# Kernel tuning notes

Hardware: AMD Instinct MI355X
Metric: run time of the kernel (lower is better)

## Reference

```python
import jax, jax.numpy as jnp
import numpy as np

N, IN_DIM, H, ATT_DIM, OUT_DIM = 4096, 512, 8, 64, 64
ATT_BIAS = 0.5


def setup_inputs() -> dict:
    key = jax.random.key(0)
    ks = jax.random.split(key, 12)
    s_in = 1.0 / np.sqrt(IN_DIM)
    s_o = 1.0 / np.sqrt(H * OUT_DIM)
    return {
        "Q": jax.random.normal(ks[0], (N, IN_DIM), jnp.float32),
        "K": jax.random.normal(ks[1], (N, IN_DIM), jnp.float32),
        "V": jax.random.normal(ks[2], (N, IN_DIM), jnp.float32),
        "adj": jax.random.uniform(ks[3], (N, N), jnp.float32),
        "WQ": jax.random.normal(ks[4], (IN_DIM, H * ATT_DIM), jnp.float32) * s_in,
        "bQ": jnp.zeros((H * ATT_DIM,), jnp.float32),
        "WK": jax.random.normal(ks[5], (IN_DIM, H * ATT_DIM), jnp.float32) * s_in,
        "bK": jnp.zeros((H * ATT_DIM,), jnp.float32),
        "WV": jax.random.normal(ks[6], (IN_DIM, H * OUT_DIM), jnp.float32) * s_in,
        "bV": jnp.zeros((H * OUT_DIM,), jnp.float32),
        "WO": jax.random.normal(ks[7], (H * OUT_DIM, OUT_DIM), jnp.float32) * s_o,
        "bO": jnp.zeros((OUT_DIM,), jnp.float32),
    }


def reference(Q, K, V, adj, WQ, bQ, WK, bK, WV, bV, WO, bO):
    scale = ATT_DIM ** -0.5
    q = (Q @ WQ + bQ).reshape(N, H, ATT_DIM)   # [N,H,d]
    k = (K @ WK + bK).reshape(N, H, ATT_DIM)   # [N,H,d]
    v = (V @ WV + bV).reshape(N, H, OUT_DIM)   # [N,H,e]
    # scaled QK^T per head: [H,N,N]
    scores = jnp.einsum("nhd,mhd->hnm", q * scale, k)
    # sigmoid -> bias subtract -> +0.1*adj -> softmax over keys
    scores = jax.nn.sigmoid(scores) - ATT_BIAS + 0.1 * adj[None, :, :]
    attn = jax.nn.softmax(scores, axis=2)
    # attend values (dropout p=0 => identity), concat heads, project
    out = jnp.einsum("hnm,mhe->nhe", attn, v).reshape(N, H * OUT_DIM)
    return out @ WO + bO
```

## Files before the change

kernel.cpp:

```cpp
#include <hip/hip_runtime.h>
#include <hip/hip_bf16.h>

#define N_TOK  4096
#define HD     512
#define NH     8
#define NSPLIT 4
#define QBLK   128
#define NT     ((N_TOK / NSPLIT) / 64)

typedef short v8s __attribute__((ext_vector_type(8)));
typedef float v4f __attribute__((ext_vector_type(4)));
typedef float v16f __attribute__((ext_vector_type(16)));
typedef unsigned short u16;

#define QSCALE   0.18033688011112042f
#define ADJ2     0.14426950408889634f
#define EA0 0.999410f
#define EA1 1.016220f
#define EA2 0.423120f
#define EA3 0.279120f

__device__ __forceinline__ float bf2f(u16 x) {
  union { unsigned int u; float f; } c; c.u = ((unsigned int)x) << 16; return c.f;
}
__device__ __forceinline__ u16 f2bf(float f) {
  union { float f; unsigned int u; } c; c.f = f;
  return (u16)((c.u + 0x7fffu + ((c.u >> 16) & 1u)) >> 16);
}
__device__ __forceinline__ float fast_exp2(float x) {
#if __has_builtin(__builtin_amdgcn_exp2f)
  return __builtin_amdgcn_exp2f(x);
#else
  return exp2f(x);
#endif
}
__device__ __forceinline__ unsigned int pk_bf16(float a, float b) {
  union { __hip_bfloat162 h; unsigned int u; } c;
  c.h = __float22bfloat162_rn(make_float2(a, b));
  return c.u;
}

typedef __attribute__((address_space(1))) const char gchar;
typedef __attribute__((address_space(3))) char lchar;
__device__ __forceinline__ void glds16(const void* g, void* l) {
  __builtin_amdgcn_global_load_lds((gchar*)g, (lchar*)l, 16, 0, 0);
}
__device__ __forceinline__ void plswap(unsigned int& a, unsigned int& b) {
  asm volatile("v_permlane32_swap_b32 %0, %1" : "+v"(a), "+v"(b));
}

__device__ __forceinline__ bool detect_f32(const u16* __restrict__ q) {
  int l = threadIdx.x & 63;
  u16 e = q[2 * l];
  float x = bf2f(e);
  int ex = (e >> 7) & 0xFF;
  float ax = fabsf(x);
  bool ok = (ex != 0xFF) && (ax < 64.f) && (ax > 1e-30f);
  unsigned long long m = __ballot(ok);
  return __popcll(m) < 48;
}
__device__ __forceinline__ float bias_ld(const void* b, int i, bool f32) {
  return f32 ? ((const float*)b)[i] : bf2f(((const u16*)b)[i]);
}

__global__ __launch_bounds__(256) void conv_adjE_k(const void* __restrict__ adj, u16* __restrict__ adjE,
                                                   const u16* __restrict__ Qdet) {
  bool f32 = detect_f32(Qdet);
  int i = blockIdx.x * 256 + threadIdx.x;
  float4 f;
  if (f32) {
    f = ((const float4*)adj)[i];
  } else {
    short4 v = ((const short4*)adj)[i];
    f.x = bf2f((u16)v.x); f.y = bf2f((u16)v.y); f.z = bf2f((u16)v.z); f.w = bf2f((u16)v.w);
  }
  unsigned int d0 = pk_bf16(fast_exp2(f.x * ADJ2), fast_exp2(f.y * ADJ2));
  unsigned int d1 = pk_bf16(fast_exp2(f.z * ADJ2), fast_exp2(f.w * ADJ2));
  ((uint2*)adjE)[i] = make_uint2(d0, d1);
}

__global__ __launch_bounds__(256) void tr_w_k(const void* W0, const void* W1, const void* W2, const void* W3,
                                              u16* t0, u16* t1, u16* t2, u16* t3,
                                              const u16* __restrict__ Qdet) {
  bool f32 = detect_f32(Qdet);
  int z = blockIdx.z;
  const void* in; u16* out; int C;
  if (z == 0)      { in = W0; out = t0; C = 512; }
  else if (z == 1) { in = W1; out = t1; C = 512; }
  else if (z == 2) { in = W2; out = t2; C = 512; }
  else             { in = W3; out = t3; C = 64; if (blockIdx.y) return; }
  const int R = 512;
  __shared__ __align__(16) u16 tile[64][72];
  const int r0 = blockIdx.x * 64, c0 = blockIdx.y * 64;
  const int t = threadIdx.x;
#pragma unroll
  for (int rep = 0; rep < 2; ++rep) {
    int idx = (t + rep * 256) * 8;
    int r = idx >> 6, c = idx & 63;
    if (f32) {
      const float* sp = (const float*)in + (size_t)(r0 + r) * C + (c0 + c);
      float4 a = *(const float4*)sp, b = *(const float4*)(sp + 4);
      uint4 q = make_uint4(pk_bf16(a.x, a.y), pk_bf16(a.z, a.w),
                           pk_bf16(b.x, b.y), pk_bf16(b.z, b.w));
      *(uint4*)&tile[r][c] = q;
    } else {
      *(v8s*)&tile[r][c] = *(const v8s*)((const u16*)in + (size_t)(r0 + r) * C + (c0 + c));
    }
  }
  __syncthreads();
#pragma unroll
  for (int rep = 0; rep < 2; ++rep) {
    int idx = (t + rep * 256) * 8;
    int oc = idx >> 6, orr = idx & 63;
    u16 tmp[8];
#pragma unroll
    for (int j = 0; j < 8; ++j) tmp[j] = tile[orr + j][oc];
    *(v8s*)(out + (size_t)(c0 + oc) * R + (r0 + orr)) = *(v8s*)tmp;
  }
}

__global__ __launch_bounds__(256) void gemm_qkv_k(const void* A0, const void* A1, const void* A2,
                                                  const u16* __restrict__ t0, const u16* __restrict__ t1,
                                                  const u16* __restrict__ t2,
                                                  const void* b0, const void* b1, const void* b2,
                                                  u16* __restrict__ qb, u16* __restrict__ kb,
                                                  u16* __restrict__ vtb) {
  __shared__ __align__(16) u16 As[64][72];
  __shared__ __align__(16) u16 Bs[64][72];
  bool f32 = detect_f32((const u16*)A0);
  int z = blockIdx.z;
  const void* Araw = (z == 0) ? A0 : (z == 1) ? A1 : A2;
  const u16* Bt    = (z == 0) ? t0 : (z == 1) ? t1 : t2;
  const void* bias = (z == 0) ? b0 : (z == 1) ? b1 : b2;
  const bool vt = (z == 2);
  const int i0 = blockIdx.x * 64, j0 = blockIdx.y * 64;
  const int t = threadIdx.x, w = t >> 6, l = t & 63, quad = l >> 4, l15 = l & 15;
  v4f acc[4] = {};
  for (int k0 = 0; k0 < 512; k0 += 64) {
#pragma unroll
    for (int rep = 0; rep < 2; ++rep) {
      int idx = (t + rep * 256) * 8;
      int r = idx >> 6, c = idx & 63;
      if (f32) {
        const float* sp = (const float*)Araw + (size_t)(i0 + r) * 512 + k0 + c;
        float4 fa = *(const float4*)sp, fb = *(const float4*)(sp + 4);
        uint4 q = make_uint4(pk_bf16(fa.x, fa.y), pk_bf16(fa.z, fa.w),
                             pk_bf16(fb.x, fb.y), pk_bf16(fb.z, fb.w));
        *(uint4*)&As[r][c] = q;
      } else {
        *(v8s*)&As[r][c] = *(const v8s*)((const u16*)Araw + (size_t)(i0 + r) * 512 + k0 + c);
      }
      *(v8s*)&Bs[r][c] = *(const v8s*)(Bt + (size_t)(j0 + r) * 512 + k0 + c);
    }
    __syncthreads();
    if (vt) {
#pragma unroll
      for (int h = 0; h < 2; ++h) {
        v8s a = *(const v8s*)&As[w * 16 + l15][h * 32 + quad * 8];
#pragma unroll
        for (int cb = 0; cb < 4; ++cb) {
          v8s b = *(const v8s*)&Bs[cb * 16 + l15][h * 32 + quad * 8];
          acc[cb] = __builtin_amdgcn_mfma_f32_16x16x32_bf16(b, a, acc[cb], 0, 0, 0);
        }
      }
    } else {
#pragma unroll
      for (int h = 0; h < 2; ++h) {
        v8s a = *(const v8s*)&As[w * 16 + l15][h * 32 + quad * 8];
#pragma unroll
        for (int cb = 0; cb < 4; ++cb) {
          v8s b = *(const v8s*)&Bs[cb * 16 + l15][h * 32 + quad * 8];
          acc[cb] = __builtin_amdgcn_mfma_f32_16x16x32_bf16(a, b, acc[cb], 0, 0, 0);
        }
      }
    }
    __syncthreads();
  }
  if (vt) {
#pragma unroll
    for (int cb = 0; cb < 4; ++cb) {
#pragma unroll
      for (int r = 0; r < 4; ++r) {
        int jj = j0 + cb * 16 + quad * 4 + r;
        int ii = i0 + w * 16 + l15;
        vtb[(size_t)jj * N_TOK + ii] = f2bf(acc[cb][r] + bias_ld(bias, jj, f32));
      }
    }
  } else {
    const float oscale = (z == 0) ? QSCALE : 1.0f;
    u16* C = (z == 0) ? qb : kb;
#pragma unroll
    for (int cb = 0; cb < 4; ++cb) {
      int col = j0 + cb * 16 + l15;
      float bv = bias_ld(bias, col, f32);
#pragma unroll
      for (int r = 0; r < 4; ++r) {
        int row = i0 + w * 16 + quad * 4 + r;
        C[(size_t)row * HD + col] = f2bf((acc[cb][r] + bv) * oscale);
      }
    }
  }
}

__global__ __launch_bounds__(256, 4) void attn_kernel(const u16* __restrict__ qb, const u16* __restrict__ kb,
                                                      const u16* __restrict__ vtb, const u16* __restrict__ adjE,
                                                      u16* __restrict__ Opart, float* __restrict__ Lpart) {
  __shared__ __align__(16) u16 Ks[2][64 * 64];
  __shared__ __align__(16) u16 Vs[2][64 * 64];
  const int i0 = blockIdx.x * QBLK, h64 = blockIdx.y * 64, z = blockIdx.z;
  const int t = threadIdx.x, w = t >> 6, l = t & 63;
  const int il = l & 31, h2 = l >> 5, il7 = il & 7;
  const int iRow = i0 + w * 32 + il;

  v8s qf[4];
#pragma unroll
  for (int c = 0; c < 4; ++c)
    qf[c] = *(const v8s*)(qb + (size_t)iRow * HD + h64 + 16 * c + 8 * h2);

  const u16* adjRow = adjE + (size_t)iRow * N_TOK + 4 * h2;

  const int srow = l >> 3;
  const int scol = ((l & 7) ^ srow) * 8;
  const int ldsrow = 16 * w;

  v16f oacc0 = {}, oacc1 = {};
  float lsum = 0.f;
  const int m_begin = z * (N_TOK / NSPLIT);

#pragma unroll
  for (int n = 0; n < 2; ++n) {
    int r = ldsrow + 8 * n + srow;
    glds16(kb + (size_t)(m_begin + r) * HD + h64 + scol, &Ks[0][(ldsrow + 8 * n) * 64]);
    glds16(vtb + (size_t)(h64 + r) * N_TOK + m_begin + scol, &Vs[0][(ldsrow + 8 * n) * 64]);
  }
  __syncthreads();

  int buf = 0;
  for (int mt = 0; mt < NT; ++mt) {
    const int m0 = m_begin + mt * 64;
    if (mt + 1 < NT) {
      const int m1 = m0 + 64;
#pragma unroll
      for (int n = 0; n < 2; ++n) {
        int r = ldsrow + 8 * n + srow;
        glds16(kb + (size_t)(m1 + r) * HD + h64 + scol, &Ks[buf ^ 1][(ldsrow + 8 * n) * 64]);
        glds16(vtb + (size_t)(h64 + r) * N_TOK + m1 + scol, &Vs[buf ^ 1][(ldsrow + 8 * n) * 64]);
      }
    }
    const u16* Kb = &Ks[buf][0];
    const u16* Vb = &Vs[buf][0];

#pragma unroll
    for (int mh = 0; mh < 2; ++mh) {
      uint2 av[4];
#pragma unroll
      for (int rq = 0; rq < 4; ++rq)
        av[rq] = *(const uint2*)(adjRow + m0 + 32 * mh + 8 * rq);

      v16f macc = {};
      __builtin_amdgcn_s_setprio(1);
#pragma unroll
      for (int c = 0; c < 4; ++c) {
        v8s kf = *(const v8s*)(Kb + (32 * mh + il) * 64 + (((2 * c + h2) ^ il7) * 8));
        macc = __builtin_amdgcn_mfma_f32_32x32x16_bf16(kf, qf[c], macc, 0, 0, 0);
      }
      __builtin_amdgcn_s_setprio(0);

      float p[16];
#pragma unroll
      for (int rq = 0; rq < 4; ++rq) {
        union { unsigned int u; float f; } e0, e1, e2, e3;
        e0.u = av[rq].x << 16; e1.u = av[rq].x & 0xFFFF0000u;
        e2.u = av[rq].y << 16; e3.u = av[rq].y & 0xFFFF0000u;
        float r0 = __builtin_amdgcn_rcpf(1.f + fast_exp2(-macc[4 * rq + 0]));
        float r1 = __builtin_amdgcn_rcpf(1.f + fast_exp2(-macc[4 * rq + 1]));
        float r2 = __builtin_amdgcn_rcpf(1.f + fast_exp2(-macc[4 * rq + 2]));
        float r3 = __builtin_amdgcn_rcpf(1.f + fast_exp2(-macc[4 * rq + 3]));
        float p0 = e0.f * fmaf(fmaf(fmaf(EA3, r0, EA2), r0, EA1), r0, EA0);
        float p1 = e1.f * fmaf(fmaf(fmaf(EA3, r1, EA2), r1, EA1), r1, EA0);
        float p2 = e2.f * fmaf(fmaf(fmaf(EA3, r2, EA2), r2, EA1), r2, EA0);
        float p3 = e3.f * fmaf(fmaf(fmaf(EA3, r3, EA2), r3, EA1), r3, EA0);
        lsum += (p0 + p1) + (p2 + p3);
        p[4 * rq + 0] = p0; p[4 * rq + 1] = p1; p[4 * rq + 2] = p2; p[4 * rq + 3] = p3;
      }

      v8s pf[2];
#pragma unroll
      for (int sub = 0; sub < 2; ++sub) {
        unsigned int u0 = pk_bf16(p[8 * sub + 0], p[8 * sub + 1]);
        unsigned int u1 = pk_bf16(p[8 * sub + 2], p[8 * sub + 3]);
        unsigned int u2 = pk_bf16(p[8 * sub + 4], p[8 * sub + 5]);
        unsigned int u3 = pk_bf16(p[8 * sub + 6], p[8 * sub + 7]);
        plswap(u0, u2); plswap(u1, u3);
        union { uint4 q; v8s v; } pu;
        pu.q = make_uint4(u0, u1, u2, u3);
        pf[sub] = pu.v;
      }

      __builtin_amdgcn_s_setprio(1);
#pragma unroll
      for (int sub = 0; sub < 2; ++sub) {
        const int mc = 2 * mh + sub;
        v8s vf0 = *(const v8s*)(Vb + (il) * 64      + (((2 * mc + h2) ^ il7) * 8));
        v8s vf1 = *(const v8s*)(Vb + (32 + il) * 64 + (((2 * mc + h2) ^ il7) * 8));
        oacc0 = __builtin_amdgcn_mfma_f32_32x32x16_bf16(pf[sub], vf0, oacc0, 0, 0, 0);
        oacc1 = __builtin_amdgcn_mfma_f32_32x32x16_bf16(pf[sub], vf1, oacc1, 0, 0, 0);
      }
      __builtin_amdgcn_s_setprio(0);
    }
    __syncthreads();
    buf ^= 1;
  }

  lsum += __shfl_xor(lsum, 32);
  if (l < 32)
    Lpart[((size_t)z * N_TOK + i0 + 32 * w + il) * NH + blockIdx.y] = lsum;

#pragma unroll
  for (int r = 0; r < 16; ++r) {
    int i_local = (r & 3) + 8 * (r >> 2) + 4 * h2;
    size_t row = (size_t)z * N_TOK + i0 + 32 * w + i_local;
    u16* op = Opart + row * HD + h64 + il;
    op[0]  = f2bf(oacc0[r]);
    op[32] = f2bf(oacc1[r]);
  }
}

__global__ __launch_bounds__(256) void gemm_bt(const u16* __restrict__ Opart, const float* __restrict__ Lpart,
                                               const u16* __restrict__ Bt, const void* bias,
                                               void* __restrict__ C, const u16* __restrict__ Qdet) {
  __shared__ __align__(16) u16 As[64][72];
  __shared__ __align__(16) u16 Bs[64][72];
  bool f32 = detect_f32(Qdet);
  const int i0 = blockIdx.x * 64;
  const int t = threadIdx.x, w = t >> 6, l = t & 63, quad = l >> 4, l15 = l & 15;
  v4f acc[4] = {};
  for (int k0 = 0; k0 < 512; k0 += 64) {
    const int h = k0 >> 6;
#pragma unroll
    for (int rep = 0; rep < 2; ++rep) {
      int idx = (t + rep * 256) * 8;
      int r = idx >> 6, c = idx & 63;
      float lv = 0.f;
#pragma unroll
      for (int s = 0; s < NSPLIT; ++s) lv += Lpart[((size_t)s * N_TOK + i0 + r) * NH + h];
      float rl = __builtin_amdgcn_rcpf(lv);
      float vals[8] = {};
#pragma unroll
      for (int s = 0; s < NSPLIT; ++s) {
        v8s ov = *(const v8s*)(Opart + ((size_t)s * N_TOK + i0 + r) * HD + k0 + c);
#pragma unroll
        for (int j = 0; j < 8; ++j) vals[j] += bf2f((u16)ov[j]);
      }
      uint4 q = make_uint4(pk_bf16(vals[0] * rl, vals[1] * rl), pk_bf16(vals[2] * rl, vals[3] * rl),
                           pk_bf16(vals[4] * rl, vals[5] * rl), pk_bf16(vals[6] * rl, vals[7] * rl));
      *(uint4*)&As[r][c] = q;
      *(v8s*)&Bs[r][c] = *(const v8s*)(Bt + (size_t)r * 512 + k0 + c);
    }
    __syncthreads();
#pragma unroll
    for (int h2 = 0; h2 < 2; ++h2) {
      v8s a = *(const v8s*)&As[w * 16 + l15][h2 * 32 + quad * 8];
#pragma unroll
      for (int cb = 0; cb < 4; ++cb) {
        v8s b = *(const v8s*)&Bs[cb * 16 + l15][h2 * 32 + quad * 8];
        acc[cb] = __builtin_amdgcn_mfma_f32_16x16x32_bf16(a, b, acc[cb], 0, 0, 0);
      }
    }
    __syncthreads();
  }
#pragma unroll
  for (int cb = 0; cb < 4; ++cb) {
    int col = cb * 16 + l15;
    float bv = bias_ld(bias, col, f32);
#pragma unroll
    for (int r = 0; r < 4; ++r) {
      int row = i0 + w * 16 + quad * 4 + r;
      float v = acc[cb][r] + bv;
      size_t idx = (size_t)row * 64 + col;
      if (f32) ((float*)C)[idx] = v;
      else     ((u16*)C)[idx] = f2bf(v);
    }
  }
}

extern "C" void kernel_launch(void* const* d_in, const int* in_sizes, int n_in,
                              void* d_out, int out_size, void* d_ws, size_t ws_size,
                              hipStream_t stream) {
  (void)in_sizes; (void)n_in; (void)out_size; (void)ws_size;
  const void* Q   = d_in[0];
  const void* K   = d_in[1];
  const void* V   = d_in[2];
  const void* adj = d_in[3];
  const void* WQ  = d_in[4];
  const void* bQ  = d_in[5];
  const void* WK  = d_in[6];
  const void* bK  = d_in[7];
  const void* WV  = d_in[8];
  const void* bV  = d_in[9];
  const void* WO  = d_in[10];
  const void* bO  = d_in[11];
  const u16* Qdet = (const u16*)Q;

  char* p = (char*)d_ws;
  auto alloc = [&](size_t bytes) { char* r = p; p += (bytes + 255) & ~(size_t)255; return r; };
  const size_t SZ = (size_t)N_TOK * HD * 2;

  u16* adjE    = (u16*)alloc((size_t)N_TOK * N_TOK * 2);
  u16* qb      = (u16*)alloc(SZ);
  u16* kb      = (u16*)alloc(SZ);
  u16* vtb     = (u16*)alloc(SZ);
  u16* Opart   = (u16*)alloc((size_t)NSPLIT * SZ);
  float* Lpart = (float*)alloc((size_t)NSPLIT * N_TOK * NH * 4);
  u16* tQ      = (u16*)alloc((size_t)512 * 512 * 2);
  u16* tK      = (u16*)alloc((size_t)512 * 512 * 2);
  u16* tV      = (u16*)alloc((size_t)512 * 512 * 2);
  u16* tO      = (u16*)alloc((size_t)64 * 512 * 2);

  dim3 b256(256);
  conv_adjE_k<<<dim3(16384), b256, 0, stream>>>(adj, adjE, Qdet);
  tr_w_k<<<dim3(8, 8, 4), b256, 0, stream>>>(WQ, WK, WV, WO, tQ, tK, tV, tO, Qdet);
  gemm_qkv_k<<<dim3(64, 8, 3), b256, 0, stream>>>(Q, K, V, tQ, tK, tV,
                                                  bQ, bK, bV, qb, kb, vtb);
  attn_kernel<<<dim3(N_TOK / QBLK, NH, NSPLIT), b256, 0, stream>>>(qb, kb, vtb, adjE, Opart, Lpart);
  gemm_bt<<<dim3(64, 1), b256, 0, stream>>>(Opart, Lpart, tO, bO, d_out, Qdet);
}
```

Before: 263.9 us.

## Fuse adjacency exp conversion into attention kernel and software-pipeline tile phases

Removes the separate pre-pass that converted adj into a bf16 exp2 table and instead reads raw adj (fp32 or bf16) directly inside the attention kernel. The kernel computes exp2(L2E*sigmoid + adj*ADJ2) with a real exp instead of the polynomial times a precomputed exp. The tile loop is restructured so K fragments, adj values and V fragments are loaded ahead and the two 32-key halves interleave. The intent is to avoid the extra pass writing and reading a 32 MB table. In exchange each of the 8 head blocks rereads fp32 adj, doubling adj bytes per read, and occupancy drops to 3 waves per SIMD.

```diff
diff --git a/kernel.cpp b/kernel.cpp
--- a/kernel.cpp
+++ b/kernel.cpp
@@ -15,10 +15,7 @@
 
 #define QSCALE   0.18033688011112042f
 #define ADJ2     0.14426950408889634f
-#define EA0 0.999410f
-#define EA1 1.016220f
-#define EA2 0.423120f
-#define EA3 0.279120f
+#define L2E      1.4426950408889634f
 
 __device__ __forceinline__ float bf2f(u16 x) {
   union { unsigned int u; float f; } c; c.u = ((unsigned int)x) << 16; return c.f;
@@ -61,22 +58,6 @@
 }
 __device__ __forceinline__ float bias_ld(const void* b, int i, bool f32) {
   return f32 ? ((const float*)b)[i] : bf2f(((const u16*)b)[i]);
-}
-
-__global__ __launch_bounds__(256) void conv_adjE_k(const void* __restrict__ adj, u16* __restrict__ adjE,
-                                                   const u16* __restrict__ Qdet) {
-  bool f32 = detect_f32(Qdet);
-  int i = blockIdx.x * 256 + threadIdx.x;
-  float4 f;
-  if (f32) {
-    f = ((const float4*)adj)[i];
-  } else {
-    short4 v = ((const short4*)adj)[i];
-    f.x = bf2f((u16)v.x); f.y = bf2f((u16)v.y); f.z = bf2f((u16)v.z); f.w = bf2f((u16)v.w);
-  }
-  unsigned int d0 = pk_bf16(fast_exp2(f.x * ADJ2), fast_exp2(f.y * ADJ2));
-  unsigned int d1 = pk_bf16(fast_exp2(f.z * ADJ2), fast_exp2(f.w * ADJ2));
-  ((uint2*)adjE)[i] = make_uint2(d0, d1);
 }
 
 __global__ __launch_bounds__(256) void tr_w_k(const void* W0, const void* W1, const void* W2, const void* W3,
@@ -202,11 +183,52 @@
   }
 }
 
-__global__ __launch_bounds__(256, 4) void attn_kernel(const u16* __restrict__ qb, const u16* __restrict__ kb,
-                                                      const u16* __restrict__ vtb, const u16* __restrict__ adjE,
+__device__ __forceinline__ void ew_phase(const v16f& macc, const uint4* av, bool f32m,
+                                         float& lsum, v8s* pf) {
+  unsigned int ua[8];
+#pragma unroll
+  for (int rq = 0; rq < 4; ++rq) {
+    float a0, a1, a2, a3;
+    if (f32m) {
+      union { unsigned int u; float f; } c0, c1, c2, c3;
+      c0.u = av[rq].x; c1.u = av[rq].y; c2.u = av[rq].z; c3.u = av[rq].w;
+      a0 = c0.f * ADJ2; a1 = c1.f * ADJ2; a2 = c2.f * ADJ2; a3 = c3.f * ADJ2;
+    } else {
+      union { unsigned int u; float f; } e0, e1, e2, e3;
+      e0.u = av[rq].x << 16; e1.u = av[rq].x & 0xFFFF0000u;
+      e2.u = av[rq].y << 16; e3.u = av[rq].y & 0xFFFF0000u;
+      a0 = e0.f * ADJ2; a1 = e1.f * ADJ2; a2 = e2.f * ADJ2; a3 = e3.f * ADJ2;
+    }
+    float r0 = __builtin_amdgcn_rcpf(1.f + fast_exp2(-macc[4 * rq + 0]));
+    float r1 = __builtin_amdgcn_rcpf(1.f + fast_exp2(-macc[4 * rq + 1]));
+    float r2 = __builtin_amdgcn_rcpf(1.f + fast_exp2(-macc[4 * rq + 2]));
+    float r3 = __builtin_amdgcn_rcpf(1.f + fast_exp2(-macc[4 * rq + 3]));
+    float p0 = fast_exp2(fmaf(L2E, r0, a0));
+    float p1 = fast_exp2(fmaf(L2E, r1, a1));
+    float p2 = fast_exp2(fmaf(L2E, r2, a2));
+    float p3 = fast_exp2(fmaf(L2E, r3, a3));
+    lsum += (p0 + p1) + (p2 + p3);
+    ua[2 * rq]     = pk_bf16(p0, p1);
+    ua[2 * rq + 1] = pk_bf16(p2, p3);
+  }
+#pragma unroll
+  for (int sub = 0; sub < 2; ++sub) {
+    unsigned int u0 = ua[4 * sub + 0], u1 = ua[4 * sub + 1];
+    unsigned int u2 = ua[4 * sub + 2], u3 = ua[4 * sub + 3];
+    plswap(u0, u2); plswap(u1, u3);
+    union { uint4 q; v8s v; } pu;
+    pu.q = make_uint4(u0, u1, u2, u3);
+    pf[sub] = pu.v;
+  }
+}
+
+__global__ __launch_bounds__(256, 3) void attn_kernel(const u16* __restrict__ qb, const u16* __restrict__ kb,
+                                                      const u16* __restrict__ vtb, const void* __restrict__ adj,
+                                                      const u16* __restrict__ Qdet,
                                                       u16* __restrict__ Opart, float* __restrict__ Lpart) {
   __shared__ __align__(16) u16 Ks[2][64 * 64];
   __shared__ __align__(16) u16 Vs[2][64 * 64];
+  const bool f32m = detect_f32(Qdet);
   const int i0 = blockIdx.x * QBLK, h64 = blockIdx.y * 64, z = blockIdx.z;
   const int t = threadIdx.x, w = t >> 6, l = t & 63;
   const int il = l & 31, h2 = l >> 5, il7 = il & 7;
@@ -217,7 +239,8 @@
   for (int c = 0; c < 4; ++c)
     qf[c] = *(const v8s*)(qb + (size_t)iRow * HD + h64 + 16 * c + 8 * h2);
 
-  const u16* adjRow = adjE + (size_t)iRow * N_TOK + 4 * h2;
+  const float* aRowF = (const float*)adj + (size_t)iRow * N_TOK + 4 * h2;
+  const u16*   aRowH = (const u16*)adj  + (size_t)iRow * N_TOK + 4 * h2;
 
   const int srow = l >> 3;
   const int scol = ((l & 7) ^ srow) * 8;
@@ -238,6 +261,31 @@
   int buf = 0;
   for (int mt = 0; mt < NT; ++mt) {
     const int m0 = m_begin + mt * 64;
+    const u16* Kb = &Ks[buf][0];
+    const u16* Vb = &Vs[buf][0];
+
+    v8s kfA[4];
+#pragma unroll
+    for (int c = 0; c < 4; ++c)
+      kfA[c] = *(const v8s*)(Kb + il * 64 + (((2 * c + h2) ^ il7) * 8));
+
+    uint4 av0[4], av1[4];
+    if (f32m) {
+#pragma unroll
+      for (int rq = 0; rq < 4; ++rq) {
+        av0[rq] = *(const uint4*)(aRowF + m0 + 8 * rq);
+        av1[rq] = *(const uint4*)(aRowF + m0 + 32 + 8 * rq);
+      }
+    } else {
+#pragma unroll
+      for (int rq = 0; rq < 4; ++rq) {
+        uint2 t0 = *(const uint2*)(aRowH + m0 + 8 * rq);
+        uint2 t1 = *(const uint2*)(aRowH + m0 + 32 + 8 * rq);
+        av0[rq].x = t0.x; av0[rq].y = t0.y; av0[rq].z = 0; av0[rq].w = 0;
+        av1[rq].x = t1.x; av1[rq].y = t1.y; av1[rq].z = 0; av1[rq].w = 0;
+      }
+    }
+
     if (mt + 1 < NT) {
       const int m1 = m0 + 64;
 #pragma unroll
@@ -247,67 +295,57 @@
         glds16(vtb + (size_t)(h64 + r) * N_TOK + m1 + scol, &Vs[buf ^ 1][(ldsrow + 8 * n) * 64]);
       }
     }
-    const u16* Kb = &Ks[buf][0];
-    const u16* Vb = &Vs[buf][0];
-
-#pragma unroll
-    for (int mh = 0; mh < 2; ++mh) {
-      uint2 av[4];
-#pragma unroll
-      for (int rq = 0; rq < 4; ++rq)
-        av[rq] = *(const uint2*)(adjRow + m0 + 32 * mh + 8 * rq);
-
-      v16f macc = {};
-      __builtin_amdgcn_s_setprio(1);
-#pragma unroll
-      for (int c = 0; c < 4; ++c) {
-        v8s kf = *(const v8s*)(Kb + (32 * mh + il) * 64 + (((2 * c + h2) ^ il7) * 8));
-        macc = __builtin_amdgcn_mfma_f32_32x32x16_bf16(kf, qf[c], macc, 0, 0, 0);
-      }
-      __builtin_amdgcn_s_setprio(0);
-
-      float p[16];
-#pragma unroll
-      for (int rq = 0; rq < 4; ++rq) {
-        union { unsigned int u; float f; } e0, e1, e2, e3;
-        e0.u = av[rq].x << 16; e1.u = av[rq].x & 0xFFFF0000u;
-        e2.u = av[rq].y << 16; e3.u = av[rq].y & 0xFFFF0000u;
-        float r0 = __builtin_amdgcn_rcpf(1.f + fast_exp2(-macc[4 * rq + 0]));
-        float r1 = __builtin_amdgcn_rcpf(1.f + fast_exp2(-macc[4 * rq + 1]));
-        float r2 = __builtin_amdgcn_rcpf(1.f + fast_exp2(-macc[4 * rq + 2]));
-        float r3 = __builtin_amdgcn_rcpf(1.f + fast_exp2(-macc[4 * rq + 3]));
-        float p0 = e0.f * fmaf(fmaf(fmaf(EA3, r0, EA2), r0, EA1), r0, EA0);
-        float p1 = e1.f * fmaf(fmaf(fmaf(EA3, r1, EA2), r1, EA1), r1, EA0);
-        float p2 = e2.f * fmaf(fmaf(fmaf(EA3, r2, EA2), r2, EA1), r2, EA0);
-        float p3 = e3.f * fmaf(fmaf(fmaf(EA3, r3, EA2), r3, EA1), r3, EA0);
-        lsum += (p0 + p1) + (p2 + p3);
-        p[4 * rq + 0] = p0; p[4 * rq + 1] = p1; p[4 * rq + 2] = p2; p[4 * rq + 3] = p3;
-      }
-
-      v8s pf[2];
-#pragma unroll
-      for (int sub = 0; sub < 2; ++sub) {
-        unsigned int u0 = pk_bf16(p[8 * sub + 0], p[8 * sub + 1]);
-        unsigned int u1 = pk_bf16(p[8 * sub + 2], p[8 * sub + 3]);
-        unsigned int u2 = pk_bf16(p[8 * sub + 4], p[8 * sub + 5]);
-        unsigned int u3 = pk_bf16(p[8 * sub + 6], p[8 * sub + 7]);
-        plswap(u0, u2); plswap(u1, u3);
-        union { uint4 q; v8s v; } pu;
-        pu.q = make_uint4(u0, u1, u2, u3);
-        pf[sub] = pu.v;
-      }
-
-      __builtin_amdgcn_s_setprio(1);
-#pragma unroll
-      for (int sub = 0; sub < 2; ++sub) {
-        const int mc = 2 * mh + sub;
-        v8s vf0 = *(const v8s*)(Vb + (il) * 64      + (((2 * mc + h2) ^ il7) * 8));
-        v8s vf1 = *(const v8s*)(Vb + (32 + il) * 64 + (((2 * mc + h2) ^ il7) * 8));
-        oacc0 = __builtin_amdgcn_mfma_f32_32x32x16_bf16(pf[sub], vf0, oacc0, 0, 0, 0);
-        oacc1 = __builtin_amdgcn_mfma_f32_32x32x16_bf16(pf[sub], vf1, oacc1, 0, 0, 0);
-      }
-      __builtin_amdgcn_s_setprio(0);
-    }
+
+    v16f macc = {};
+    __builtin_amdgcn_s_setprio(1);
+#pragma unroll
+    for (int c = 0; c < 4; ++c)
+      macc = __builtin_amdgcn_mfma_f32_32x32x16_bf16(kfA[c], qf[c], macc, 0, 0, 0);
+    __builtin_amdgcn_s_setprio(0);
+
+    v8s kfB[4];
+#pragma unroll
+    for (int c = 0; c < 4; ++c)
+      kfB[c] = *(const v8s*)(Kb + (32 + il) * 64 + (((2 * c + h2) ^ il7) * 8));
+    v8s vf[4];
+#pragma unroll
+    for (int sub = 0; sub < 2; ++sub) {
+      vf[2 * sub]     = *(const v8s*)(Vb + il * 64        + (((2 * sub + h2) ^ il7) * 8));
+      vf[2 * sub + 1] = *(const v8s*)(Vb + (32 + il) * 64 + (((2 * sub + h2) ^ il7) * 8));
+    }
+
+    v8s pf[2];
+    ew_phase(macc, av0, f32m, lsum, pf);
+    __builtin_amdgcn_s_setprio(1);
+#pragma unroll
+    for (int sub = 0; sub < 2; ++sub) {
+      oacc0 = __builtin_amdgcn_mfma_f32_32x32x16_bf16(pf[sub], vf[2 * sub], oacc0, 0, 0, 0);
+      oacc1 = __builtin_amdgcn_mfma_f32_32x32x16_bf16(pf[sub], vf[2 * sub + 1], oacc1, 0, 0, 0);
+    }
+    __builtin_amdgcn_s_setprio(0);
+
+    v16f macc2 = {};
+    __builtin_amdgcn_s_setprio(1);
+#pragma unroll
+    for (int c = 0; c < 4; ++c)
+      macc2 = __builtin_amdgcn_mfma_f32_32x32x16_bf16(kfB[c], qf[c], macc2, 0, 0, 0);
+    __builtin_amdgcn_s_setprio(0);
+
+#pragma unroll
+    for (int sub = 0; sub < 2; ++sub) {
+      vf[2 * sub]     = *(const v8s*)(Vb + il * 64        + (((2 * (2 + sub) + h2) ^ il7) * 8));
+      vf[2 * sub + 1] = *(const v8s*)(Vb + (32 + il) * 64 + (((2 * (2 + sub) + h2) ^ il7) * 8));
+    }
+
+    ew_phase(macc2, av1, f32m, lsum, pf);
+    __builtin_amdgcn_s_setprio(1);
+#pragma unroll
+    for (int sub = 0; sub < 2; ++sub) {
+      oacc0 = __builtin_amdgcn_mfma_f32_32x32x16_bf16(pf[sub], vf[2 * sub], oacc0, 0, 0, 0);
+      oacc1 = __builtin_amdgcn_mfma_f32_32x32x16_bf16(pf[sub], vf[2 * sub + 1], oacc1, 0, 0, 0);
+    }
+    __builtin_amdgcn_s_setprio(0);
+
     __syncthreads();
     buf ^= 1;
   }
@@ -406,7 +444,6 @@
   auto alloc = [&](size_t bytes) { char* r = p; p += (bytes + 255) & ~(size_t)255; return r; };
   const size_t SZ = (size_t)N_TOK * HD * 2;
 
-  u16* adjE    = (u16*)alloc((size_t)N_TOK * N_TOK * 2);
   u16* qb      = (u16*)alloc(SZ);
   u16* kb      = (u16*)alloc(SZ);
   u16* vtb     = (u16*)alloc(SZ);
@@ -418,10 +455,9 @@
   u16* tO      = (u16*)alloc((size_t)64 * 512 * 2);
 
   dim3 b256(256);
-  conv_adjE_k<<<dim3(16384), b256, 0, stream>>>(adj, adjE, Qdet);
   tr_w_k<<<dim3(8, 8, 4), b256, 0, stream>>>(WQ, WK, WV, WO, tQ, tK, tV, tO, Qdet);
   gemm_qkv_k<<<dim3(64, 8, 3), b256, 0, stream>>>(Q, K, V, tQ, tK, tV,
                                                   bQ, bK, bV, qb, kb, vtb);
-  attn_kernel<<<dim3(N_TOK / QBLK, NH, NSPLIT), b256, 0, stream>>>(qb, kb, vtb, adjE, Opart, Lpart);
+  attn_kernel<<<dim3(N_TOK / QBLK, NH, NSPLIT), b256, 0, stream>>>(qb, kb, vtb, adj, Qdet, Opart, Lpart);
   gemm_bt<<<dim3(64, 1), b256, 0, stream>>>(Opart, Lpart, tO, bO, d_out, Qdet);
 }
```

After: 363.1 us. 37.6% more time.

## Deepen attention split, prefetch adjacency with explicit vmcnt pipeline, separate combine kernel

Applied to the files above, without the earlier changes.

Doubles the key-dimension split so the attention grid has twice as many blocks. The attention loop is restructured into a two-stage software pipeline: adjacency loads are prefetched into registers along with the K/V LDS loads, and hand-placed vmcnt waits and barriers replace the old per-tile syncthreads. The split-combine and normalisation move out of the 64-block output GEMM into a wide standalone combine kernel. This aims to hide global-load latency and raise parallelism, at the cost of more partial-output traffic, an extra launch and more register pressure.

```diff
diff --git a/kernel.cpp b/kernel.cpp
--- a/kernel.cpp
+++ b/kernel.cpp
@@ -4,7 +4,7 @@
 #define N_TOK  4096
 #define HD     512
 #define NH     8
-#define NSPLIT 4
+#define NSPLIT 8
 #define QBLK   128
 #define NT     ((N_TOK / NSPLIT) / 64)
 
@@ -48,6 +48,9 @@
 __device__ __forceinline__ void plswap(unsigned int& a, unsigned int& b) {
   asm volatile("v_permlane32_swap_b32 %0, %1" : "+v"(a), "+v"(b));
 }
+#define WAIT12 asm volatile("s_waitcnt vmcnt(12)" ::: "memory")
+#define WAIT0  asm volatile("s_waitcnt vmcnt(0)" ::: "memory")
+#define SBAR   __builtin_amdgcn_s_barrier()
 
 __device__ __forceinline__ bool detect_f32(const u16* __restrict__ q) {
   int l = threadIdx.x & 63;
@@ -202,6 +205,63 @@
   }
 }
 
+__device__ __forceinline__ void tile_compute(const u16* __restrict__ Kb, const u16* __restrict__ Vb,
+                                             const uint2* av, const v8s* qf,
+                                             v16f& oacc0, v16f& oacc1, float& lsum,
+                                             int il, int h2, int il7) {
+#pragma unroll
+  for (int mh = 0; mh < 2; ++mh) {
+    v16f macc = {};
+    __builtin_amdgcn_s_setprio(1);
+#pragma unroll
+    for (int c = 0; c < 4; ++c) {
+      v8s kf = *(const v8s*)(Kb + (32 * mh + il) * 64 + (((2 * c + h2) ^ il7) * 8));
+      macc = __builtin_amdgcn_mfma_f32_32x32x16_bf16(kf, qf[c], macc, 0, 0, 0);
+    }
+    __builtin_amdgcn_s_setprio(0);
+
+    unsigned int ua[8];
+#pragma unroll
+    for (int rq = 0; rq < 4; ++rq) {
+      uint2 a = av[4 * mh + rq];
+      union { unsigned int u; float f; } e0, e1, e2, e3;
+      e0.u = a.x << 16; e1.u = a.x & 0xFFFF0000u;
+      e2.u = a.y << 16; e3.u = a.y & 0xFFFF0000u;
+      float r0 = __builtin_amdgcn_rcpf(1.f + fast_exp2(-macc[4 * rq + 0]));
+      float r1 = __builtin_amdgcn_rcpf(1.f + fast_exp2(-macc[4 * rq + 1]));
+      float r2 = __builtin_amdgcn_rcpf(1.f + fast_exp2(-macc[4 * rq + 2]));
+      float r3 = __builtin_amdgcn_rcpf(1.f + fast_exp2(-macc[4 * rq + 3]));
+      float p0 = e0.f * fmaf(fmaf(fmaf(EA3, r0, EA2), r0, EA1), r0, EA0);
+      float p1 = e1.f * fmaf(fmaf(fmaf(EA3, r1, EA2), r1, EA1), r1, EA0);
+      float p2 = e2.f * fmaf(fmaf(fmaf(EA3, r2, EA2), r2, EA1), r2, EA0);
+      float p3 = e3.f * fmaf(fmaf(fmaf(EA3, r3, EA2), r3, EA1), r3, EA0);
+      lsum += (p0 + p1) + (p2 + p3);
+      ua[2 * rq]     = pk_bf16(p0, p1);
+      ua[2 * rq + 1] = pk_bf16(p2, p3);
+    }
+    v8s pf[2];
+#pragma unroll
+    for (int sub = 0; sub < 2; ++sub) {
+      unsigned int u0 = ua[4 * sub + 0], u1 = ua[4 * sub + 1];
+      unsigned int u2 = ua[4 * sub + 2], u3 = ua[4 * sub + 3];
+      plswap(u0, u2); plswap(u1, u3);
+      union { uint4 q; v8s v; } pu;
+      pu.q = make_uint4(u0, u1, u2, u3);
+      pf[sub] = pu.v;
+    }
+    __builtin_amdgcn_s_setprio(1);
+#pragma unroll
+    for (int sub = 0; sub < 2; ++sub) {
+      const int mc = 2 * mh + sub;
+      v8s vf0 = *(const v8s*)(Vb + il * 64        + (((2 * mc + h2) ^ il7) * 8));
+      v8s vf1 = *(const v8s*)(Vb + (32 + il) * 64 + (((2 * mc + h2) ^ il7) * 8));
+      oacc0 = __builtin_amdgcn_mfma_f32_32x32x16_bf16(pf[sub], vf0, oacc0, 0, 0, 0);
+      oacc1 = __builtin_amdgcn_mfma_f32_32x32x16_bf16(pf[sub], vf1, oacc1, 0, 0, 0);
+    }
+    __builtin_amdgcn_s_setprio(0);
+  }
+}
+
 __global__ __launch_bounds__(256, 4) void attn_kernel(const u16* __restrict__ qb, const u16* __restrict__ kb,
                                                       const u16* __restrict__ vtb, const u16* __restrict__ adjE,
                                                       u16* __restrict__ Opart, float* __restrict__ Lpart) {
@@ -215,7 +275,7 @@
   v8s qf[4];
 #pragma unroll
   for (int c = 0; c < 4; ++c)
-    qf[c] = *(const v8s*)(qb + (size_t)iRow * HD + h64 + 16 * c + 8 * h2);
+    qf[c] = *(const v8s*)(qb + (size_t)iRow * HD + 16 * c + 8 * h2 + h64);
 
   const u16* adjRow = adjE + (size_t)iRow * N_TOK + 4 * h2;
 
@@ -223,94 +283,61 @@
   const int scol = ((l & 7) ^ srow) * 8;
   const int ldsrow = 16 * w;
 
+#define ADJLD(AV, MM)                                                        \
+  _Pragma("unroll") for (int q_ = 0; q_ < 8; ++q_)                           \
+      AV[q_] = *(const uint2*)(adjRow + (MM) + 32 * (q_ >> 2) + 8 * (q_ & 3));
+#define STAGE(KB, VB, MM)                                                    \
+  _Pragma("unroll") for (int n_ = 0; n_ < 2; ++n_) {                         \
+    int r_ = ldsrow + 8 * n_ + srow;                                         \
+    glds16(kb + (size_t)((MM) + r_) * HD + h64 + scol,                       \
+           (u16*)(KB) + (ldsrow + 8 * n_) * 64);                             \
+    glds16(vtb + (size_t)(h64 + r_) * N_TOK + (MM) + scol,                   \
+           (u16*)(VB) + (ldsrow + 8 * n_) * 64);                             \
+  }
+
   v16f oacc0 = {}, oacc1 = {};
   float lsum = 0.f;
   const int m_begin = z * (N_TOK / NSPLIT);
-
-#pragma unroll
-  for (int n = 0; n < 2; ++n) {
-    int r = ldsrow + 8 * n + srow;
-    glds16(kb + (size_t)(m_begin + r) * HD + h64 + scol, &Ks[0][(ldsrow + 8 * n) * 64]);
-    glds16(vtb + (size_t)(h64 + r) * N_TOK + m_begin + scol, &Vs[0][(ldsrow + 8 * n) * 64]);
-  }
-  __syncthreads();
-
-  int buf = 0;
-  for (int mt = 0; mt < NT; ++mt) {
-    const int m0 = m_begin + mt * 64;
-    if (mt + 1 < NT) {
-      const int m1 = m0 + 64;
-#pragma unroll
-      for (int n = 0; n < 2; ++n) {
-        int r = ldsrow + 8 * n + srow;
-        glds16(kb + (size_t)(m1 + r) * HD + h64 + scol, &Ks[buf ^ 1][(ldsrow + 8 * n) * 64]);
-        glds16(vtb + (size_t)(h64 + r) * N_TOK + m1 + scol, &Vs[buf ^ 1][(ldsrow + 8 * n) * 64]);
-      }
-    }
-    const u16* Kb = &Ks[buf][0];
-    const u16* Vb = &Vs[buf][0];
-
-#pragma unroll
-    for (int mh = 0; mh < 2; ++mh) {
-      uint2 av[4];
-#pragma unroll
-      for (int rq = 0; rq < 4; ++rq)
-        av[rq] = *(const uint2*)(adjRow + m0 + 32 * mh + 8 * rq);
-
-      v16f macc = {};
-      __builtin_amdgcn_s_setprio(1);
-#pragma unroll
-      for (int c = 0; c < 4; ++c) {
-        v8s kf = *(const v8s*)(Kb + (32 * mh + il) * 64 + (((2 * c + h2) ^ il7) * 8));
-        macc = __builtin_amdgcn_mfma_f32_32x32x16_bf16(kf, qf[c], macc, 0, 0, 0);
-      }
-      __builtin_amdgcn_s_setprio(0);
-
-      float p[16];
-#pragma unroll
-      for (int rq = 0; rq < 4; ++rq) {
-        union { unsigned int u; float f; } e0, e1, e2, e3;
-        e0.u = av[rq].x << 16; e1.u = av[rq].x & 0xFFFF0000u;
-        e2.u = av[rq].y << 16; e3.u = av[rq].y & 0xFFFF0000u;
-        float r0 = __builtin_amdgcn_rcpf(1.f + fast_exp2(-macc[4 * rq + 0]));
-        float r1 = __builtin_amdgcn_rcpf(1.f + fast_exp2(-macc[4 * rq + 1]));
-        float r2 = __builtin_amdgcn_rcpf(1.f + fast_exp2(-macc[4 * rq + 2]));
-        float r3 = __builtin_amdgcn_rcpf(1.f + fast_exp2(-macc[4 * rq + 3]));
-        float p0 = e0.f * fmaf(fmaf(fmaf(EA3, r0, EA2), r0, EA1), r0, EA0);
-        float p1 = e1.f * fmaf(fmaf(fmaf(EA3, r1, EA2), r1, EA1), r1, EA0);
-        float p2 = e2.f * fmaf(fmaf(fmaf(EA3, r2, EA2), r2, EA1), r2, EA0);
-        float p3 = e3.f * fmaf(fmaf(fmaf(EA3, r3, EA2), r3, EA1), r3, EA0);
-        lsum += (p0 + p1) + (p2 + p3);
-        p[4 * rq + 0] = p0; p[4 * rq + 1] = p1; p[4 * rq + 2] = p2; p[4 * rq + 3] = p3;
-      }
-
-      v8s pf[2];
-#pragma unroll
-      for (int sub = 0; sub < 2; ++sub) {
-        unsigned int u0 = pk_bf16(p[8 * sub + 0], p[8 * sub + 1]);
-        unsigned int u1 = pk_bf16(p[8 * sub + 2], p[8 * sub + 3]);
-        unsigned int u2 = pk_bf16(p[8 * sub + 4], p[8 * sub + 5]);
-        unsigned int u3 = pk_bf16(p[8 * sub + 6], p[8 * sub + 7]);
-        plswap(u0, u2); plswap(u1, u3);
-        union { uint4 q; v8s v; } pu;
-        pu.q = make_uint4(u0, u1, u2, u3);
-        pf[sub] = pu.v;
-      }
-
-      __builtin_amdgcn_s_setprio(1);
-#pragma unroll
-      for (int sub = 0; sub < 2; ++sub) {
-        const int mc = 2 * mh + sub;
-        v8s vf0 = *(const v8s*)(Vb + (il) * 64      + (((2 * mc + h2) ^ il7) * 8));
-        v8s vf1 = *(const v8s*)(Vb + (32 + il) * 64 + (((2 * mc + h2) ^ il7) * 8));
-        oacc0 = __builtin_amdgcn_mfma_f32_32x32x16_bf16(pf[sub], vf0, oacc0, 0, 0, 0);
-        oacc1 = __builtin_amdgcn_mfma_f32_32x32x16_bf16(pf[sub], vf1, oacc1, 0, 0, 0);
-      }
-      __builtin_amdgcn_s_setprio(0);
-    }
-    __syncthreads();
-    buf ^= 1;
-  }
+  uint2 avA[8], avB[8];
+
+  ADJLD(avA, m_begin)
+  STAGE(Ks[0], Vs[0], m_begin)
+  ADJLD(avB, m_begin + 64)
+  STAGE(Ks[1], Vs[1], m_begin + 64)
+  WAIT12;
+  SBAR;
+  __builtin_amdgcn_sched_barrier(0);
+
+  for (int mt = 0; mt < NT; mt += 2) {
+    const int m2 = m_begin + (mt + 2) * 64;
+    const int m3 = m_begin + (mt + 3) * 64;
+
+    tile_compute(Ks[0], Vs[0], avA, qf, oacc0, oacc1, lsum, il, h2, il7);
+    SBAR;
+    if (mt + 2 < NT) {
+      ADJLD(avA, m2)
+      STAGE(Ks[0], Vs[0], m2)
+      WAIT12;
+    } else {
+      WAIT0;
+    }
+    SBAR;
+    __builtin_amdgcn_sched_barrier(0);
+
+    tile_compute(Ks[1], Vs[1], avB, qf, oacc0, oacc1, lsum, il, h2, il7);
+    SBAR;
+    if (mt + 3 < NT) {
+      ADJLD(avB, m3)
+      STAGE(Ks[1], Vs[1], m3)
+      WAIT12;
+    } else {
+      WAIT0;
+    }
+    SBAR;
+    __builtin_amdgcn_sched_barrier(0);
+  }
+#undef ADJLD
+#undef STAGE
 
   lsum += __shfl_xor(lsum, 32);
   if (l < 32)
@@ -326,9 +353,29 @@
   }
 }
 
-__global__ __launch_bounds__(256) void gemm_bt(const u16* __restrict__ Opart, const float* __restrict__ Lpart,
-                                               const u16* __restrict__ Bt, const void* bias,
-                                               void* __restrict__ C, const u16* __restrict__ Qdet) {
+__global__ __launch_bounds__(256) void combine_k(const u16* __restrict__ Opart, const float* __restrict__ Lpart,
+                                                 u16* __restrict__ Oc) {
+  int id = blockIdx.x * 256 + threadIdx.x;
+  int row = id >> 6, v = id & 63, h = v >> 3;
+  float L = 0.f;
+#pragma unroll
+  for (int s = 0; s < NSPLIT; ++s) L += Lpart[((size_t)s * N_TOK + row) * NH + h];
+  float rl = __builtin_amdgcn_rcpf(L);
+  float vals[8] = {};
+#pragma unroll
+  for (int s = 0; s < NSPLIT; ++s) {
+    v8s ov = *(const v8s*)(Opart + ((size_t)s * N_TOK + row) * HD + v * 8);
+#pragma unroll
+    for (int j = 0; j < 8; ++j) vals[j] += bf2f((u16)ov[j]);
+  }
+  uint4 q = make_uint4(pk_bf16(vals[0] * rl, vals[1] * rl), pk_bf16(vals[2] * rl, vals[3] * rl),
+                       pk_bf16(vals[4] * rl, vals[5] * rl), pk_bf16(vals[6] * rl, vals[7] * rl));
+  *(uint4*)(Oc + (size_t)id * 8) = q;
+}
+
+__global__ __launch_bounds__(256) void gemm_bt(const u16* __restrict__ Oc, const u16* __restrict__ Bt,
+                                               const void* bias, void* __restrict__ C,
+                                               const u16* __restrict__ Qdet) {
   __shared__ __align__(16) u16 As[64][72];
   __shared__ __align__(16) u16 Bs[64][72];
   bool f32 = detect_f32(Qdet);
@@ -336,25 +383,11 @@
   const int t = threadIdx.x, w = t >> 6, l = t & 63, quad = l >> 4, l15 = l & 15;
   v4f acc[4] = {};
   for (int k0 = 0; k0 < 512; k0 += 64) {
-    const int h = k0 >> 6;
 #pragma unroll
     for (int rep = 0; rep < 2; ++rep) {
       int idx = (t + rep * 256) * 8;
       int r = idx >> 6, c = idx & 63;
-      float lv = 0.f;
-#pragma unroll
-      for (int s = 0; s < NSPLIT; ++s) lv += Lpart[((size_t)s * N_TOK + i0 + r) * NH + h];
-      float rl = __builtin_amdgcn_rcpf(lv);
-      float vals[8] = {};
-#pragma unroll
-      for (int s = 0; s < NSPLIT; ++s) {
-        v8s ov = *(const v8s*)(Opart + ((size_t)s * N_TOK + i0 + r) * HD + k0 + c);
-#pragma unroll
-        for (int j = 0; j < 8; ++j) vals[j] += bf2f((u16)ov[j]);
-      }
-      uint4 q = make_uint4(pk_bf16(vals[0] * rl, vals[1] * rl), pk_bf16(vals[2] * rl, vals[3] * rl),
-                           pk_bf16(vals[4] * rl, vals[5] * rl), pk_bf16(vals[6] * rl, vals[7] * rl));
-      *(uint4*)&As[r][c] = q;
+      *(v8s*)&As[r][c] = *(const v8s*)(Oc + (size_t)(i0 + r) * 512 + k0 + c);
       *(v8s*)&Bs[r][c] = *(const v8s*)(Bt + (size_t)r * 512 + k0 + c);
     }
     __syncthreads();
@@ -411,6 +444,7 @@
   u16* kb      = (u16*)alloc(SZ);
   u16* vtb     = (u16*)alloc(SZ);
   u16* Opart   = (u16*)alloc((size_t)NSPLIT * SZ);
+  u16* Oc      = (u16*)alloc(SZ);
   float* Lpart = (float*)alloc((size_t)NSPLIT * N_TOK * NH * 4);
   u16* tQ      = (u16*)alloc((size_t)512 * 512 * 2);
   u16* tK      = (u16*)alloc((size_t)512 * 512 * 2);
@@ -423,5 +457,6 @@
   gemm_qkv_k<<<dim3(64, 8, 3), b256, 0, stream>>>(Q, K, V, tQ, tK, tV,
                                                   bQ, bK, bV, qb, kb, vtb);
   attn_kernel<<<dim3(N_TOK / QBLK, NH, NSPLIT), b256, 0, stream>>>(qb, kb, vtb, adjE, Opart, Lpart);
-  gemm_bt<<<dim3(64, 1), b256, 0, stream>>>(Opart, Lpart, tO, bO, d_out, Qdet);
-}
+  combine_k<<<dim3(1024), b256, 0, stream>>>(Opart, Lpart, Oc);
+  gemm_bt<<<dim3(64, 1), b256, 0, stream>>>(Oc, tO, bO, d_out, Qdet);
+}
```

New measurement: 411.0 us. 55.7% more time.

## Process two 32-row query tiles per wave to reuse K/V LDS fragments

Applied to the files above, without the earlier changes.

Doubles the query block per workgroup from 128 to 256 rows, so each wave handles two 32-row query tiles sharing the same K and V fragments read from LDS. This halves K/V global-to-LDS traffic and LDS fragment reads per unit of work and interleaves two independent MFMA chains. The cost is higher register pressure: four output accumulators and two score accumulators, with launch bounds lowered from 4 to 2 waves per SIMD. There are also half as many workgroups in the grid.

```diff
diff --git a/kernel.cpp b/kernel.cpp
--- a/kernel.cpp
+++ b/kernel.cpp
@@ -5,7 +5,7 @@
 #define HD     512
 #define NH     8
 #define NSPLIT 4
-#define QBLK   128
+#define QBLK   256
 #define NT     ((N_TOK / NSPLIT) / 64)
 
 typedef short v8s __attribute__((ext_vector_type(8)));
@@ -202,7 +202,39 @@
   }
 }
 
-__global__ __launch_bounds__(256, 4) void attn_kernel(const u16* __restrict__ qb, const u16* __restrict__ kb,
+__device__ __forceinline__ void ew_pack(const v16f& macc, uint2 A0, uint2 A1, uint2 A2, uint2 A3,
+                                        float& lsum, v8s& pf0, v8s& pf1) {
+  unsigned int ua0, ua1, ua2, ua3, ua4, ua5, ua6, ua7;
+#define EW4(A, R, UA, UB)                                                       \
+  {                                                                             \
+    union { unsigned int u; float f; } e0, e1, e2, e3;                          \
+    e0.u = (A).x << 16; e1.u = (A).x & 0xFFFF0000u;                             \
+    e2.u = (A).y << 16; e3.u = (A).y & 0xFFFF0000u;                             \
+    float r0 = __builtin_amdgcn_rcpf(1.f + fast_exp2(-macc[(R) + 0]));          \
+    float r1 = __builtin_amdgcn_rcpf(1.f + fast_exp2(-macc[(R) + 1]));          \
+    float r2 = __builtin_amdgcn_rcpf(1.f + fast_exp2(-macc[(R) + 2]));          \
+    float r3 = __builtin_amdgcn_rcpf(1.f + fast_exp2(-macc[(R) + 3]));          \
+    float p0 = e0.f * fmaf(fmaf(fmaf(EA3, r0, EA2), r0, EA1), r0, EA0);         \
+    float p1 = e1.f * fmaf(fmaf(fmaf(EA3, r1, EA2), r1, EA1), r1, EA0);         \
+    float p2 = e2.f * fmaf(fmaf(fmaf(EA3, r2, EA2), r2, EA1), r2, EA0);         \
+    float p3 = e3.f * fmaf(fmaf(fmaf(EA3, r3, EA2), r3, EA1), r3, EA0);         \
+    lsum += (p0 + p1) + (p2 + p3);                                              \
+    UA = pk_bf16(p0, p1); UB = pk_bf16(p2, p3);                                 \
+  }
+  EW4(A0, 0,  ua0, ua1)
+  EW4(A1, 4,  ua2, ua3)
+  EW4(A2, 8,  ua4, ua5)
+  EW4(A3, 12, ua6, ua7)
+#undef EW4
+  plswap(ua0, ua2); plswap(ua1, ua3);
+  plswap(ua4, ua6); plswap(ua5, ua7);
+  union { uint4 q; v8s v; } p0, p1;
+  p0.q = make_uint4(ua0, ua1, ua2, ua3);
+  p1.q = make_uint4(ua4, ua5, ua6, ua7);
+  pf0 = p0.v; pf1 = p1.v;
+}
+
+__global__ __launch_bounds__(256, 2) void attn_kernel(const u16* __restrict__ qb, const u16* __restrict__ kb,
                                                       const u16* __restrict__ vtb, const u16* __restrict__ adjE,
                                                       u16* __restrict__ Opart, float* __restrict__ Lpart) {
   __shared__ __align__(16) u16 Ks[2][64 * 64];
@@ -210,21 +242,25 @@
   const int i0 = blockIdx.x * QBLK, h64 = blockIdx.y * 64, z = blockIdx.z;
   const int t = threadIdx.x, w = t >> 6, l = t & 63;
   const int il = l & 31, h2 = l >> 5, il7 = il & 7;
-  const int iRow = i0 + w * 32 + il;
-
-  v8s qf[4];
-#pragma unroll
-  for (int c = 0; c < 4; ++c)
-    qf[c] = *(const v8s*)(qb + (size_t)iRow * HD + h64 + 16 * c + 8 * h2);
-
-  const u16* adjRow = adjE + (size_t)iRow * N_TOK + 4 * h2;
+  const int iRowA = i0 + w * 64 + il;
+  const int iRowB = iRowA + 32;
+
+  v8s qfA[4], qfB[4];
+#pragma unroll
+  for (int c = 0; c < 4; ++c) {
+    qfA[c] = *(const v8s*)(qb + (size_t)iRowA * HD + h64 + 16 * c + 8 * h2);
+    qfB[c] = *(const v8s*)(qb + (size_t)iRowB * HD + h64 + 16 * c + 8 * h2);
+  }
+
+  const u16* adjRowA = adjE + (size_t)iRowA * N_TOK + 4 * h2;
+  const u16* adjRowB = adjE + (size_t)iRowB * N_TOK + 4 * h2;
 
   const int srow = l >> 3;
   const int scol = ((l & 7) ^ srow) * 8;
   const int ldsrow = 16 * w;
 
-  v16f oacc0 = {}, oacc1 = {};
-  float lsum = 0.f;
+  v16f oaccA0 = {}, oaccA1 = {}, oaccB0 = {}, oaccB1 = {};
+  float lsumA = 0.f, lsumB = 0.f;
   const int m_begin = z * (N_TOK / NSPLIT);
 
 #pragma unroll
@@ -252,59 +288,39 @@
 
 #pragma unroll
     for (int mh = 0; mh < 2; ++mh) {
-      uint2 av[4];
-#pragma unroll
-      for (int rq = 0; rq < 4; ++rq)
-        av[rq] = *(const uint2*)(adjRow + m0 + 32 * mh + 8 * rq);
-
-      v16f macc = {};
+      uint2 avA[4], avB[4];
+#pragma unroll
+      for (int rq = 0; rq < 4; ++rq) {
+        avA[rq] = *(const uint2*)(adjRowA + m0 + 32 * mh + 8 * rq);
+        avB[rq] = *(const uint2*)(adjRowB + m0 + 32 * mh + 8 * rq);
+      }
+
+      v16f maccA = {}, maccB = {};
       __builtin_amdgcn_s_setprio(1);
 #pragma unroll
       for (int c = 0; c < 4; ++c) {
         v8s kf = *(const v8s*)(Kb + (32 * mh + il) * 64 + (((2 * c + h2) ^ il7) * 8));
-        macc = __builtin_amdgcn_mfma_f32_32x32x16_bf16(kf, qf[c], macc, 0, 0, 0);
+        maccA = __builtin_amdgcn_mfma_f32_32x32x16_bf16(kf, qfA[c], maccA, 0, 0, 0);
+        maccB = __builtin_amdgcn_mfma_f32_32x32x16_bf16(kf, qfB[c], maccB, 0, 0, 0);
       }
       __builtin_amdgcn_s_setprio(0);
 
-      float p[16];
-#pragma unroll
-      for (int rq = 0; rq < 4; ++rq) {
-        union { unsigned int u; float f; } e0, e1, e2, e3;
-        e0.u = av[rq].x << 16; e1.u = av[rq].x & 0xFFFF0000u;
-        e2.u = av[rq].y << 16; e3.u = av[rq].y & 0xFFFF0000u;
-        float r0 = __builtin_amdgcn_rcpf(1.f + fast_exp2(-macc[4 * rq + 0]));
-        float r1 = __builtin_amdgcn_rcpf(1.f + fast_exp2(-macc[4 * rq + 1]));
-        float r2 = __builtin_amdgcn_rcpf(1.f + fast_exp2(-macc[4 * rq + 2]));
-        float r3 = __builtin_amdgcn_rcpf(1.f + fast_exp2(-macc[4 * rq + 3]));
-        float p0 = e0.f * fmaf(fmaf(fmaf(EA3, r0, EA2), r0, EA1), r0, EA0);
-        float p1 = e1.f * fmaf(fmaf(fmaf(EA3, r1, EA2), r1, EA1), r1, EA0);
-        float p2 = e2.f * fmaf(fmaf(fmaf(EA3, r2, EA2), r2, EA1), r2, EA0);
-        float p3 = e3.f * fmaf(fmaf(fmaf(EA3, r3, EA2), r3, EA1), r3, EA0);
-        lsum += (p0 + p1) + (p2 + p3);
-        p[4 * rq + 0] = p0; p[4 * rq + 1] = p1; p[4 * rq + 2] = p2; p[4 * rq + 3] = p3;
-      }
-
-      v8s pf[2];
-#pragma unroll
-      for (int sub = 0; sub < 2; ++sub) {
-        unsigned int u0 = pk_bf16(p[8 * sub + 0], p[8 * sub + 1]);
-        unsigned int u1 = pk_bf16(p[8 * sub + 2], p[8 * sub + 3]);
-        unsigned int u2 = pk_bf16(p[8 * sub + 4], p[8 * sub + 5]);
-        unsigned int u3 = pk_bf16(p[8 * sub + 6], p[8 * sub + 7]);
-        plswap(u0, u2); plswap(u1, u3);
-        union { uint4 q; v8s v; } pu;
-        pu.q = make_uint4(u0, u1, u2, u3);
-        pf[sub] = pu.v;
-      }
+      v8s pfA0, pfA1, pfB0, pfB1;
+      ew_pack(maccA, avA[0], avA[1], avA[2], avA[3], lsumA, pfA0, pfA1);
+      ew_pack(maccB, avB[0], avB[1], avB[2], avB[3], lsumB, pfB0, pfB1);
 
       __builtin_amdgcn_s_setprio(1);
 #pragma unroll
       for (int sub = 0; sub < 2; ++sub) {
         const int mc = 2 * mh + sub;
+        v8s pa_A = sub ? pfA1 : pfA0;
+        v8s pa_B = sub ? pfB1 : pfB0;
         v8s vf0 = *(const v8s*)(Vb + (il) * 64      + (((2 * mc + h2) ^ il7) * 8));
         v8s vf1 = *(const v8s*)(Vb + (32 + il) * 64 + (((2 * mc + h2) ^ il7) * 8));
-        oacc0 = __builtin_amdgcn_mfma_f32_32x32x16_bf16(pf[sub], vf0, oacc0, 0, 0, 0);
-        oacc1 = __builtin_amdgcn_mfma_f32_32x32x16_bf16(pf[sub], vf1, oacc1, 0, 0, 0);
+        oaccA0 = __builtin_amdgcn_mfma_f32_32x32x16_bf16(pa_A, vf0, oaccA0, 0, 0, 0);
+        oaccA1 = __builtin_amdgcn_mfma_f32_32x32x16_bf16(pa_A, vf1, oaccA1, 0, 0, 0);
+        oaccB0 = __builtin_amdgcn_mfma_f32_32x32x16_bf16(pa_B, vf0, oaccB0, 0, 0, 0);
+        oaccB1 = __builtin_amdgcn_mfma_f32_32x32x16_bf16(pa_B, vf1, oaccB1, 0, 0, 0);
       }
       __builtin_amdgcn_s_setprio(0);
     }
@@ -312,17 +328,23 @@
     buf ^= 1;
   }
 
-  lsum += __shfl_xor(lsum, 32);
-  if (l < 32)
-    Lpart[((size_t)z * N_TOK + i0 + 32 * w + il) * NH + blockIdx.y] = lsum;
+  lsumA += __shfl_xor(lsumA, 32);
+  lsumB += __shfl_xor(lsumB, 32);
+  if (l < 32) {
+    Lpart[((size_t)z * N_TOK + i0 + 64 * w + il) * NH + blockIdx.y] = lsumA;
+    Lpart[((size_t)z * N_TOK + i0 + 64 * w + 32 + il) * NH + blockIdx.y] = lsumB;
+  }
 
 #pragma unroll
   for (int r = 0; r < 16; ++r) {
     int i_local = (r & 3) + 8 * (r >> 2) + 4 * h2;
-    size_t row = (size_t)z * N_TOK + i0 + 32 * w + i_local;
-    u16* op = Opart + row * HD + h64 + il;
-    op[0]  = f2bf(oacc0[r]);
-    op[32] = f2bf(oacc1[r]);
+    size_t rowA = (size_t)z * N_TOK + i0 + 64 * w + i_local;
+    u16* opA = Opart + rowA * HD + h64 + il;
+    opA[0]  = f2bf(oaccA0[r]);
+    opA[32] = f2bf(oaccA1[r]);
+    u16* opB = opA + (size_t)32 * HD;
+    opB[0]  = f2bf(oaccB0[r]);
+    opB[32] = f2bf(oaccB1[r]);
   }
 }
 
```

New measurement: 270.8 us. 1.03x slower.
